# Performance work log

Hardware: AMD Instinct MI355X
Metric: run time of the kernel (lower is better)

Reference implementation:

```python
import jax, jax.numpy as jnp
import numpy as np
import math

N = 10000      # num nodes
DEG = 3        # base avg out-degree of random directed graph
D = 128        # d_model
H = 8          # heads
C = D // H     # head dim
L = 2          # num_layers
HOPS = 2       # num_hops


def _build_attn_window(rng):
    # random directed base graph
    E0 = N * DEG
    s0 = rng.integers(0, N, E0).astype(np.int64)
    d0 = rng.integers(0, N, E0).astype(np.int64)
    # to_undirected + coalesce
    s = np.concatenate([s0, d0]); d = np.concatenate([d0, s0])
    key = np.unique(s * N + d)
    s, d = key // N, key % N
    # add self loops (as in _get_attn_window) and coalesce
    loops = np.arange(N, dtype=np.int64)
    key = np.unique(np.concatenate([loops * N + loops, s * N + d]))
    s, d = key // N, key % N
    # base adjacency in CSR-like form grouped by source
    order = np.argsort(s, kind='stable')
    bss, bsd = s[order], d[order]
    outdeg = np.bincount(bss, minlength=N)
    indptr = np.concatenate([[0], np.cumsum(outdeg)])
    # k_hop = A; for _ in range(HOPS-1): k_hop = k_hop @ A   (boolean sparse product)
    cs, cd = s.copy(), d.copy()
    for _ in range(HOPS - 1):
        counts = outdeg[cd]
        total = int(counts.sum())
        new_s = np.repeat(cs, counts)
        starts = np.repeat(indptr[cd], counts)
        offs = np.arange(total, dtype=np.int64) - np.repeat(
            np.concatenate([[0], np.cumsum(counts)])[:-1], counts)
        new_d = bsd[starts + offs]
        key = np.unique(new_s * N + new_d)
        cs, cd = key // N, key % N
    return np.stack([cs, cd]).astype(np.int64)  # [2, E2] (src, dst)


def setup_inputs() -> dict:
    rng = np.random.default_rng(0)
    aw = _build_attn_window(rng)
    key = jax.random.key(0)
    ks = jax.random.split(key, 10)
    sc = 1.0 / math.sqrt(D)
    x = jax.random.normal(ks[0], (N, D), jnp.float32)
    Wq = jax.random.normal(ks[1], (L, D, D), jnp.float32) * sc
    Wk = jax.random.normal(ks[2], (L, D, D), jnp.float32) * sc
    Wv = jax.random.normal(ks[3], (L, D, D), jnp.float32) * sc
    Ws = jax.random.normal(ks[4], (L, D, D), jnp.float32) * sc
    bq = jax.random.normal(ks[5], (L, D), jnp.float32) * 0.01
    bk = jax.random.normal(ks[6], (L, D), jnp.float32) * 0.01
    bv = jax.random.normal(ks[7], (L, D), jnp.float32) * 0.01
    bs = jax.random.normal(ks[8], (L, D), jnp.float32) * 0.01
    return {"x": x, "Wq": Wq, "bq": bq, "Wk": Wk, "bk": bk,
            "Wv": Wv, "bv": bv, "Ws": Ws, "bs": bs,
            "attn_window": jnp.asarray(aw)}


def _segment_softmax(logits, seg):
    # logits: [E, H], seg: [E] destination node ids (every node has a self loop)
    m = jax.ops.segment_max(logits, seg, num_segments=N)
    e = jnp.exp(logits - m[seg])
    z = jax.ops.segment_sum(e, seg, num_segments=N)
    return e / z[seg]


def _transformer_conv(h, wq, bq_, wk, bk_, wv, bv_, ws, bs_, src, dst):
    # PyG TransformerConv (concat=True, root_weight=True, beta=False, eval mode)
    q = (h @ wq + bq_).reshape(N, H, C)
    k = (h @ wk + bk_).reshape(N, H, C)
    v = (h @ wv + bv_).reshape(N, H, C)
    logits = jnp.einsum('ehc,ehc->eh', q[dst], k[src]) * (1.0 / math.sqrt(C))
    alpha = _segment_softmax(logits, dst)                       # [E, H]
    agg = jax.ops.segment_sum(alpha[:, :, None] * v[src], dst,  # [N, H, C]
                              num_segments=N)
    return agg.reshape(N, D) + h @ ws + bs_


def reference(x, Wq, bq, Wk, bk, Wv, bv, Ws, bs, attn_window):
    src, dst = attn_window[0], attn_window[1]
    h = x
    for l in range(L - 1):
        h = jax.nn.relu(h + _transformer_conv(
            h, Wq[l], bq[l], Wk[l], bk[l], Wv[l], bv[l], Ws[l], bs[l], src, dst))
    l = L - 1
    h = h + _transformer_conv(
        h, Wq[l], bq[l], Wk[l], bk[l], Wv[l], bv[l], Ws[l], bs[l], src, dst)
    return h
```

## Files before the change

### kernel.cpp

```cpp
#include <hip/hip_runtime.h>
#include <hip/hip_bf16.h>

typedef __hip_bfloat16 bf16;
typedef __attribute__((ext_vector_type(8))) short bf16x8v;
typedef __attribute__((ext_vector_type(4))) float f32x4v;

#define N_NODES 10000
#define DMODEL  128
#define NHEADS  8
#define CHEAD   16


__device__ __forceinline__ float bf2f(unsigned u) {
    union { unsigned i; float f; } c; c.i = u << 16; return c.f;
}
__device__ __forceinline__ unsigned short f2bf_bits(float f) {
    bf16 b = __float2bfloat16(f);
    return *(unsigned short*)&b;
}

__global__ void build_csr(const int* __restrict__ aw, int E,
                          int* __restrict__ rowptr, int* __restrict__ nbr) {
    __shared__ int nz;
    if (threadIdx.x == 0) nz = 0;
    __syncthreads();
    int W = 4096;
    if (W > 2 * E) W = 2 * E;
    int any = 0;
    for (int w = 1 + 2 * (int)threadIdx.x; w < W; w += 2 * blockDim.x)
        any |= aw[w];
    if (any) atomicOr(&nz, 1);
    __syncthreads();
    const int is64 = (nz == 0);

    int e = blockIdx.x * blockDim.x + threadIdx.x;
    if (e == 0) rowptr[N_NODES] = E;
    if (e < E) {
        int s  = is64 ? aw[2 * e] : aw[e];
        if (s < 0) s = 0;
        if (s >= N_NODES) s = N_NODES - 1;
        int sp = (e == 0) ? -1 : (is64 ? aw[2 * (e - 1)] : aw[e - 1]);
        for (int r = sp + 1; r <= s; ++r) rowptr[r] = e;
        if (e == E - 1)
            for (int r = s + 1; r < N_NODES; ++r) rowptr[r] = E;
        int d = is64 ? aw[2 * (E + e)] : aw[E + e];
        if (d < 0) d = 0;
        if (d >= N_NODES) d = N_NODES - 1;
        nbr[e] = d;
    }
}

__global__ __launch_bounds__(256) void gemm_qkvs(
    const float* __restrict__ A,
    const float* __restrict__ Wq, const float* __restrict__ Wk,
    const float* __restrict__ Wv, const float* __restrict__ Ws,
    const float* __restrict__ bq, const float* __restrict__ bk,
    const float* __restrict__ bv, const float* __restrict__ bs,
    int welem, int belem,
    float* __restrict__ qo, bf16* __restrict__ ko, bf16* __restrict__ vo,
    float* __restrict__ hso)
{
    const int cb    = blockIdx.x;
    const int row0  = blockIdx.y * 64;
    const int col0g = cb * 64;
    const int mat   = col0g >> 7;
    const float* W    = (mat == 0) ? Wq : (mat == 1) ? Wk : (mat == 2) ? Wv : Ws;
    const float* bias = (mat == 0) ? bq : (mat == 1) ? bk : (mat == 2) ? bv : bs;
    const int colW0 = col0g & 127;

    __shared__ unsigned short As[64][136];
    __shared__ unsigned short Bs[128][68];

    const int tid = threadIdx.x;

    #pragma unroll
    for (int i = 0; i < 8; ++i) {
        int idx = tid + i * 256;
        int row = idx >> 5, k4 = idx & 31;
        int grow = row0 + row;
        float4 av = make_float4(0.f, 0.f, 0.f, 0.f);
        if (grow < N_NODES)
            av = *(const float4*)&A[grow * DMODEL + k4 * 4];
        ushort4 p;
        p.x = f2bf_bits(av.x); p.y = f2bf_bits(av.y);
        p.z = f2bf_bits(av.z); p.w = f2bf_bits(av.w);
        *(ushort4*)&As[row][k4 * 4] = p;
    }
    #pragma unroll
    for (int i = 0; i < 8; ++i) {
        int idx = tid + i * 256;
        int kk = idx >> 4, n4 = idx & 15;
        float4 wv = *(const float4*)&W[welem + kk * DMODEL + colW0 + n4 * 4];
        ushort4 p;
        p.x = f2bf_bits(wv.x); p.y = f2bf_bits(wv.y);
        p.z = f2bf_bits(wv.z); p.w = f2bf_bits(wv.w);
        *(ushort4*)&Bs[kk][n4 * 4] = p;
    }
    __syncthreads();

    const int wave = tid >> 6, lane = tid & 63;
    const int ln = lane & 15, quad = lane >> 4;
    const int ncol = wave * 16 + ln;

    f32x4v acc[4];
    #pragma unroll
    for (int mt = 0; mt < 4; ++mt) acc[mt] = (f32x4v){0.f, 0.f, 0.f, 0.f};

    #pragma unroll
    for (int ks = 0; ks < 4; ++ks) {
        const int kb = ks * 32 + quad * 8;
        bf16x8v bfv;
        #pragma unroll
        for (int j = 0; j < 8; ++j) bfv[j] = (short)Bs[kb + j][ncol];
        #pragma unroll
        for (int mt = 0; mt < 4; ++mt) {
            bf16x8v afv = *(const bf16x8v*)&As[mt * 16 + ln][kb];
            acc[mt] = __builtin_amdgcn_mfma_f32_16x16x32_bf16(afv, bfv,
                                                              acc[mt], 0, 0, 0);
        }
    }

    const float bcol = bias[belem + colW0 + ncol];
    #pragma unroll
    for (int mt = 0; mt < 4; ++mt) {
        #pragma unroll
        for (int r = 0; r < 4; ++r) {
            int row = row0 + mt * 16 + quad * 4 + r;
            if (row >= N_NODES) continue;
            float val = acc[mt][r] + bcol;
            int elo = row * DMODEL + colW0 + ncol;
            if (mat == 0)      qo[elo] = val;
            else if (mat == 3) hso[elo] = val;
            else if (mat == 1) ko[elo] = __float2bfloat16(val);
            else               vo[elo] = __float2bfloat16(val);
        }
    }
}

__global__ __launch_bounds__(256) void attn_fused(
    const float* __restrict__ q, const bf16* __restrict__ k,
    const bf16* __restrict__ v, const float* __restrict__ hs,
    const float* __restrict__ hin,
    const int* __restrict__ rowptr, const int* __restrict__ nbr,
    float* __restrict__ out, int relu_flag)
{
    const int wavesPerBlock = blockDim.x >> 6;
    const int wid = blockIdx.x * wavesPerBlock + (threadIdx.x >> 6);
    const int nWaves = gridDim.x * wavesPerBlock;
    const int l = threadIdx.x & 63;
    const int h = l & 7, slot = l >> 3;
    const int hc = l >> 3;

    for (int d = wid; d < N_NODES; d += nWaves) {
        float qf[16];
        const float* qp = q + d * DMODEL + h * CHEAD;
        #pragma unroll
        for (int i = 0; i < 4; ++i) {
            float4 t4 = *(const float4*)(qp + i * 4);
            qf[i * 4 + 0] = t4.x; qf[i * 4 + 1] = t4.y;
            qf[i * 4 + 2] = t4.z; qf[i * 4 + 3] = t4.w;
        }

        const int e0 = rowptr[d], e1 = rowptr[d + 1];
        float m_run = -3.0e38f, zacc = 0.f;
        float2 acc = make_float2(0.f, 0.f);

        for (int base = e0; base < e1; base += 8) {
            const int nedge = e1 - base;
            int s = (slot < nedge) ? nbr[base + slot] : d;
            float p = -3.0e38f;
            if (slot < nedge) {
                const uint4* kp = (const uint4*)(k + s * DMODEL + h * CHEAD);
                uint4 ka = kp[0], kb_ = kp[1];
                const unsigned* w0 = (const unsigned*)&ka;
                const unsigned* w1 = (const unsigned*)&kb_;
                float dot = 0.f;
                #pragma unroll
                for (int w = 0; w < 4; ++w) {
                    dot += qf[w * 2 + 0] * bf2f(w0[w] & 0xffffu);
                    dot += qf[w * 2 + 1] * bf2f(w0[w] >> 16);
                }
                #pragma unroll
                for (int w = 0; w < 4; ++w) {
                    dot += qf[8 + w * 2 + 0] * bf2f(w1[w] & 0xffffu);
                    dot += qf[8 + w * 2 + 1] * bf2f(w1[w] >> 16);
                }
                p = dot * 0.25f;
            }
            float gm = p;
            gm = fmaxf(gm, __shfl_xor(gm, 8));
            gm = fmaxf(gm, __shfl_xor(gm, 16));
            gm = fmaxf(gm, __shfl_xor(gm, 32));
            float mnew = fmaxf(m_run, gm);
            float scale = __expf(m_run - mnew);
            m_run = mnew;
            float pe = __expf(p - mnew);
            zacc = zacc * scale + pe;
            float scB = __shfl(scale, hc);
            acc.x *= scB; acc.y *= scB;
            int   se[8];
            float pee[8];
            #pragma unroll
            for (int e = 0; e < 8; ++e) {
                se[e]  = __shfl(s,  e * 8);
                pee[e] = __shfl(pe, e * 8 + hc);
            }
            unsigned uv[8];
            #pragma unroll
            for (int e = 0; e < 8; ++e)
                uv[e] = *(const unsigned*)(v + se[e] * DMODEL + 2 * l);
            #pragma unroll
            for (int e = 0; e < 8; ++e) {
                acc.x += pee[e] * bf2f(uv[e] & 0xffffu);
                acc.y += pee[e] * bf2f(uv[e] >> 16);
            }
        }

        float z = zacc;
        z += __shfl_xor(z, 8);
        z += __shfl_xor(z, 16);
        z += __shfl_xor(z, 32);
        float zh = __shfl(z, hc);
        float inv = (zh > 0.f) ? (1.f / zh) : 0.f;

        int idx = d * DMODEL + 2 * l;
        float2 hsv = *(const float2*)(hs + idx);
        float2 hiv = *(const float2*)(hin + idx);
        float2 o;
        o.x = acc.x * inv + hsv.x + hiv.x;
        o.y = acc.y * inv + hsv.y + hiv.y;
        if (relu_flag) { o.x = fmaxf(o.x, 0.f); o.y = fmaxf(o.y, 0.f); }
        *(float2*)(out + idx) = o;
    }
}

extern "C" void kernel_launch(void* const* d_in, const int* in_sizes, int n_in,
                              void* d_out, int out_size, void* d_ws, size_t ws_size,
                              hipStream_t stream) {
    const float* x  = (const float*)d_in[0];
    const float* Wq = (const float*)d_in[1];
    const float* bq = (const float*)d_in[2];
    const float* Wk = (const float*)d_in[3];
    const float* bk = (const float*)d_in[4];
    const float* Wv = (const float*)d_in[5];
    const float* bv = (const float*)d_in[6];
    const float* Ws = (const float*)d_in[7];
    const float* bs = (const float*)d_in[8];
    const int*   aw = (const int*)d_in[9];
    const int E = in_sizes[9] / 2;

    char* ws = (char*)d_ws;
    size_t off = 0;
    float* qb = (float*)(ws + off);  off += (size_t)N_NODES * DMODEL * 4;
    bf16*  kb = (bf16*)(ws + off);   off += (size_t)N_NODES * DMODEL * 2;
    bf16*  vb = (bf16*)(ws + off);   off += (size_t)N_NODES * DMODEL * 2;
    float* hsb = (float*)(ws + off); off += (size_t)N_NODES * DMODEL * 4;
    float* h1 = (float*)(ws + off);  off += (size_t)N_NODES * DMODEL * 4;
    int* rowptr = (int*)(ws + off);  off += ((size_t)N_NODES + 2) * 4;
    int* nbr    = (int*)(ws + off);  off += (size_t)E * 4;

    build_csr<<<(E + 255) / 256, 256, 0, stream>>>(aw, E, rowptr, nbr);

    dim3 ggrid(8, (N_NODES + 63) / 64);
    const int ablocks = (N_NODES + 3) / 4;

    gemm_qkvs<<<ggrid, 256, 0, stream>>>(x, Wq, Wk, Wv, Ws, bq, bk, bv, bs,
                                         0, 0, qb, kb, vb, hsb);
    attn_fused<<<ablocks, 256, 0, stream>>>(qb, kb, vb, hsb, x, rowptr, nbr,
                                            h1, 1);
    gemm_qkvs<<<ggrid, 256, 0, stream>>>(h1, Wq, Wk, Wv, Ws, bq, bk, bv, bs,
                                         DMODEL * DMODEL, DMODEL,
                                         qb, kb, vb, hsb);
    attn_fused<<<ablocks, 256, 0, stream>>>(qb, kb, vb, hsb, h1, rowptr, nbr,
                                            (float*)d_out, 0);
}
```

Measured before the change: 173.0 us.

## Pre-convert GEMM inputs to bf16 and prefetch next K edge batch in attention

```diff
diff --git a/kernel.cpp b/kernel.cpp
--- a/kernel.cpp
+++ b/kernel.cpp
@@ -20,7 +20,9 @@
 }
 
 __global__ void build_csr(const int* __restrict__ aw, int E,
-                          int* __restrict__ rowptr, int* __restrict__ nbr) {
+                          int* __restrict__ rowptr, int* __restrict__ nbr,
+                          const float* __restrict__ x,
+                          unsigned short* __restrict__ xb) {
     __shared__ int nz;
     if (threadIdx.x == 0) nz = 0;
     __syncthreads();
@@ -33,7 +35,21 @@
     __syncthreads();
     const int is64 = (nz == 0);
 
-    int e = blockIdx.x * blockDim.x + threadIdx.x;
+    const int gid = blockIdx.x * blockDim.x + threadIdx.x;
+    const int gtotal = gridDim.x * blockDim.x;
+
+    for (int i = gid; i < N_NODES * DMODEL / 8; i += gtotal) {
+        float4 a = *(const float4*)&x[i * 8];
+        float4 b = *(const float4*)&x[i * 8 + 4];
+        uint4 u;
+        u.x = f2bf_bits(a.x) | ((unsigned)f2bf_bits(a.y) << 16);
+        u.y = f2bf_bits(a.z) | ((unsigned)f2bf_bits(a.w) << 16);
+        u.z = f2bf_bits(b.x) | ((unsigned)f2bf_bits(b.y) << 16);
+        u.w = f2bf_bits(b.z) | ((unsigned)f2bf_bits(b.w) << 16);
+        *(uint4*)&xb[i * 8] = u;
+    }
+
+    int e = gid;
     if (e == 0) rowptr[N_NODES] = E;
     if (e < E) {
         int s  = is64 ? aw[2 * e] : aw[e];
@@ -51,7 +67,7 @@
 }
 
 __global__ __launch_bounds__(256) void gemm_qkvs(
-    const float* __restrict__ A,
+    const unsigned short* __restrict__ A,
     const float* __restrict__ Wq, const float* __restrict__ Wk,
     const float* __restrict__ Wv, const float* __restrict__ Ws,
     const float* __restrict__ bq, const float* __restrict__ bk,
@@ -74,17 +90,14 @@
     const int tid = threadIdx.x;
 
     #pragma unroll
-    for (int i = 0; i < 8; ++i) {
+    for (int i = 0; i < 4; ++i) {
         int idx = tid + i * 256;
-        int row = idx >> 5, k4 = idx & 31;
+        int row = idx >> 4, k8 = idx & 15;
         int grow = row0 + row;
-        float4 av = make_float4(0.f, 0.f, 0.f, 0.f);
+        uint4 u = make_uint4(0u, 0u, 0u, 0u);
         if (grow < N_NODES)
-            av = *(const float4*)&A[grow * DMODEL + k4 * 4];
-        ushort4 p;
-        p.x = f2bf_bits(av.x); p.y = f2bf_bits(av.y);
-        p.z = f2bf_bits(av.z); p.w = f2bf_bits(av.w);
-        *(ushort4*)&As[row][k4 * 4] = p;
+            u = *(const uint4*)&A[grow * DMODEL + k8 * 8];
+        *(uint4*)&As[row][k8 * 8] = u;
     }
     #pragma unroll
     for (int i = 0; i < 8; ++i) {
@@ -142,7 +155,8 @@
     const bf16* __restrict__ v, const float* __restrict__ hs,
     const float* __restrict__ hin,
     const int* __restrict__ rowptr, const int* __restrict__ nbr,
-    float* __restrict__ out, int relu_flag)
+    float* __restrict__ out, unsigned short* __restrict__ outb,
+    int relu_flag)
 {
     const int wavesPerBlock = blockDim.x >> 6;
     const int wid = blockIdx.x * wavesPerBlock + (threadIdx.x >> 6);
@@ -165,28 +179,42 @@
         float m_run = -3.0e38f, zacc = 0.f;
         float2 acc = make_float2(0.f, 0.f);
 
+        int eg = e0 + slot;
+        bool pad_cur = !(eg < e1);
+        int s_cur = pad_cur ? d : nbr[eg];
+        const uint4* kp0 = (const uint4*)(k + s_cur * DMODEL + h * CHEAD);
+        uint4 kc0 = kp0[0], kc1 = kp0[1];
+
         for (int base = e0; base < e1; base += 8) {
-            const int nedge = e1 - base;
-            int s = (slot < nedge) ? nbr[base + slot] : d;
-            float p = -3.0e38f;
-            if (slot < nedge) {
-                const uint4* kp = (const uint4*)(k + s * DMODEL + h * CHEAD);
-                uint4 ka = kp[0], kb_ = kp[1];
-                const unsigned* w0 = (const unsigned*)&ka;
-                const unsigned* w1 = (const unsigned*)&kb_;
-                float dot = 0.f;
-                #pragma unroll
-                for (int w = 0; w < 4; ++w) {
-                    dot += qf[w * 2 + 0] * bf2f(w0[w] & 0xffffu);
-                    dot += qf[w * 2 + 1] * bf2f(w0[w] >> 16);
-                }
-                #pragma unroll
-                for (int w = 0; w < 4; ++w) {
-                    dot += qf[8 + w * 2 + 0] * bf2f(w1[w] & 0xffffu);
-                    dot += qf[8 + w * 2 + 1] * bf2f(w1[w] >> 16);
-                }
-                p = dot * 0.25f;
+            int en = base + 8 + slot;
+            bool pad_nxt = !(en < e1);
+            int s_nxt = pad_nxt ? d : nbr[en];
+            const uint4* kpn = (const uint4*)(k + s_nxt * DMODEL + h * CHEAD);
+            uint4 kn0 = kpn[0], kn1 = kpn[1];
+
+            int se[8];
+            #pragma unroll
+            for (int e = 0; e < 8; ++e) se[e] = __shfl(s_cur, e * 8);
+            unsigned uv[8];
+            #pragma unroll
+            for (int e = 0; e < 8; ++e)
+                uv[e] = *(const unsigned*)(v + se[e] * DMODEL + 2 * l);
+
+            const unsigned* w0 = (const unsigned*)&kc0;
+            const unsigned* w1 = (const unsigned*)&kc1;
+            float dot = 0.f;
+            #pragma unroll
+            for (int w = 0; w < 4; ++w) {
+                dot += qf[w * 2 + 0] * bf2f(w0[w] & 0xffffu);
+                dot += qf[w * 2 + 1] * bf2f(w0[w] >> 16);
             }
+            #pragma unroll
+            for (int w = 0; w < 4; ++w) {
+                dot += qf[8 + w * 2 + 0] * bf2f(w1[w] & 0xffffu);
+                dot += qf[8 + w * 2 + 1] * bf2f(w1[w] >> 16);
+            }
+            float p = pad_cur ? -3.0e38f : dot * 0.25f;
+
             float gm = p;
             gm = fmaxf(gm, __shfl_xor(gm, 8));
             gm = fmaxf(gm, __shfl_xor(gm, 16));
@@ -196,24 +224,19 @@
             m_run = mnew;
             float pe = __expf(p - mnew);
             zacc = zacc * scale + pe;
+
             float scB = __shfl(scale, hc);
             acc.x *= scB; acc.y *= scB;
-            int   se[8];
             float pee[8];
             #pragma unroll
-            for (int e = 0; e < 8; ++e) {
-                se[e]  = __shfl(s,  e * 8);
-                pee[e] = __shfl(pe, e * 8 + hc);
-            }
-            unsigned uv[8];
-            #pragma unroll
-            for (int e = 0; e < 8; ++e)
-                uv[e] = *(const unsigned*)(v + se[e] * DMODEL + 2 * l);
+            for (int e = 0; e < 8; ++e) pee[e] = __shfl(pe, e * 8 + hc);
             #pragma unroll
             for (int e = 0; e < 8; ++e) {
                 acc.x += pee[e] * bf2f(uv[e] & 0xffffu);
                 acc.y += pee[e] * bf2f(uv[e] >> 16);
             }
+
+            kc0 = kn0; kc1 = kn1; s_cur = s_nxt; pad_cur = pad_nxt;
         }
 
         float z = zacc;
@@ -231,6 +254,10 @@
         o.y = acc.y * inv + hsv.y + hiv.y;
         if (relu_flag) { o.x = fmaxf(o.x, 0.f); o.y = fmaxf(o.y, 0.f); }
         *(float2*)(out + idx) = o;
+        if (outb) {
+            unsigned pk = f2bf_bits(o.x) | ((unsigned)f2bf_bits(o.y) << 16);
+            *(unsigned*)&outb[idx] = pk;
+        }
     }
 }
 
@@ -256,21 +283,28 @@
     bf16*  vb = (bf16*)(ws + off);   off += (size_t)N_NODES * DMODEL * 2;
     float* hsb = (float*)(ws + off); off += (size_t)N_NODES * DMODEL * 4;
     float* h1 = (float*)(ws + off);  off += (size_t)N_NODES * DMODEL * 4;
+    unsigned short* xbb = (unsigned short*)(ws + off);
+    off += (size_t)N_NODES * DMODEL * 2;
+    unsigned short* h1b = (unsigned short*)(ws + off);
+    off += (size_t)N_NODES * DMODEL * 2;
     int* rowptr = (int*)(ws + off);  off += ((size_t)N_NODES + 2) * 4;
     int* nbr    = (int*)(ws + off);  off += (size_t)E * 4;
 
-    build_csr<<<(E + 255) / 256, 256, 0, stream>>>(aw, E, rowptr, nbr);
+    int cblocks = (E + 255) / 256;
+    const int convBlocks = (N_NODES * DMODEL / 8 + 255) / 256;
+    if (cblocks < convBlocks) cblocks = convBlocks;
+    build_csr<<<cblocks, 256, 0, stream>>>(aw, E, rowptr, nbr, x, xbb);
 
     dim3 ggrid(8, (N_NODES + 63) / 64);
     const int ablocks = (N_NODES + 3) / 4;
 
-    gemm_qkvs<<<ggrid, 256, 0, stream>>>(x, Wq, Wk, Wv, Ws, bq, bk, bv, bs,
+    gemm_qkvs<<<ggrid, 256, 0, stream>>>(xbb, Wq, Wk, Wv, Ws, bq, bk, bv, bs,
                                          0, 0, qb, kb, vb, hsb);
     attn_fused<<<ablocks, 256, 0, stream>>>(qb, kb, vb, hsb, x, rowptr, nbr,
-                                            h1, 1);
-    gemm_qkvs<<<ggrid, 256, 0, stream>>>(h1, Wq, Wk, Wv, Ws, bq, bk, bv, bs,
+                                            h1, h1b, 1);
+    gemm_qkvs<<<ggrid, 256, 0, stream>>>(h1b, Wq, Wk, Wv, Ws, bq, bk, bv, bs,
                                          DMODEL * DMODEL, DMODEL,
                                          qb, kb, vb, hsb);
     attn_fused<<<ablocks, 256, 0, stream>>>(qb, kb, vb, hsb, h1, rowptr, nbr,
-                                            (float*)d_out, 0);
-}
+                                            (float*)d_out, (unsigned short*)0, 0);
+}
```

After: 165.6 us. 1.04x faster.
